# Kernel optimization log

Measured on AMD Instinct MI355X. Metric: run time of the kernel, lower is better.

## Reference

```python
import jax, jax.numpy as jnp
import numpy as np

N = 100000   # nodes
E = 1600000  # edges
F = 64       # input_features == output_features
BN_EPS = 1e-5


def _bn(x, gamma, beta):
    # torch BatchNorm1d (training mode): biased batch statistics
    mu = jnp.mean(x, axis=0)
    var = jnp.var(x, axis=0)
    return (x - mu) * jax.lax.rsqrt(var + BN_EPS) * gamma + beta


def setup_inputs() -> dict:
    key = jax.random.key(0)
    ks = jax.random.split(key, 16)
    s = 0.05
    inp = {
        'node_feats': jax.random.normal(ks[0], (N, F), jnp.float32),
        'edge_feats': jax.random.normal(ks[1], (E, F), jnp.float32),
        'src': jax.random.randint(ks[2], (E,), 0, N, jnp.int32),
        'dst': jax.random.randint(ks[3], (E,), 0, N, jnp.int32),
        # linear params: W [F_in, F_out], b [F_out]
        'W_src_gate': jax.random.normal(ks[4], (F, F), jnp.float32) * s,
        'b_src_gate': jnp.zeros((F,), jnp.float32),
        'W_dst_gate': jax.random.normal(ks[5], (F, F), jnp.float32) * s,
        'b_dst_gate': jnp.zeros((F,), jnp.float32),
        'W_edge_gate': jax.random.normal(ks[6], (F, F), jnp.float32) * s,
        'b_edge_gate': jnp.zeros((F,), jnp.float32),
        'W_src_update': jax.random.normal(ks[7], (F, F), jnp.float32) * s,
        'b_src_update': jnp.zeros((F,), jnp.float32),
        'W_dst_update': jax.random.normal(ks[8], (F, F), jnp.float32) * s,
        'b_dst_update': jnp.zeros((F,), jnp.float32),
        'bn_nodes_gamma': jnp.ones((F,), jnp.float32),
        'bn_nodes_beta': jnp.zeros((F,), jnp.float32),
        'bn_edges_gamma': jnp.ones((F,), jnp.float32),
        'bn_edges_beta': jnp.zeros((F,), jnp.float32),
    }
    return inp


def reference(node_feats, edge_feats, src, dst,
              W_src_gate, b_src_gate, W_dst_gate, b_dst_gate,
              W_edge_gate, b_edge_gate, W_src_update, b_src_update,
              W_dst_update, b_dst_update,
              bn_nodes_gamma, bn_nodes_beta, bn_edges_gamma, bn_edges_beta):
    # EdgeGatedGraphConv (arXiv:1711.07553), residual=True
    e_src = node_feats @ W_src_gate + b_src_gate          # [N,F]
    e_dst = node_feats @ W_dst_gate + b_dst_gate          # [N,F]
    # u_add_v gather + edge transform -> gate logits m [E,F]
    m = e_src[src] + e_dst[dst] + (edge_feats @ W_edge_gate + b_edge_gate)
    sigma = jax.nn.sigmoid(m)                             # [E,F]
    Bh = node_feats @ W_dst_update + b_dst_update         # [N,F]
    # u_mul_e message + scatter-sum to destination nodes
    sum_sigma_h = jax.ops.segment_sum(Bh[src] * sigma, dst, num_segments=node_feats.shape[0])
    sum_sigma = jax.ops.segment_sum(sigma, dst, num_segments=node_feats.shape[0])
    h = sum_sigma_h / (sum_sigma + 1e-6)                  # normalized aggregation
    x = node_feats @ W_src_update + b_src_update + h
    x = jax.nn.silu(_bn(x, bn_nodes_gamma, bn_nodes_beta))
    y = jax.nn.silu(_bn(m, bn_edges_gamma, bn_edges_beta))
    x = node_feats + x   # residual
    y = edge_feats + y   # residual
    return (x, y)
```

## Files before the change

### kernel.cpp

```cpp
#include <hip/hip_runtime.h>
#include <hip/hip_bf16.h>

typedef __attribute__((ext_vector_type(8))) __bf16 bf16x8;
typedef __attribute__((ext_vector_type(4))) float f32x4;

#define MFMA(a,b,c) __builtin_amdgcn_mfma_f32_16x16x32_bf16((a),(b),(c),0,0,0)

__device__ __forceinline__ bf16x8 cvt8(float4 a, float4 b){
  bf16x8 r;
  r[0]=(__bf16)a.x; r[1]=(__bf16)a.y; r[2]=(__bf16)a.z; r[3]=(__bf16)a.w;
  r[4]=(__bf16)b.x; r[5]=(__bf16)b.y; r[6]=(__bf16)b.z; r[7]=(__bf16)b.w;
  return r;
}

__global__ void zero_k(int4* __restrict__ p, int n4){
  int i = blockIdx.x*256 + threadIdx.x, st = gridDim.x*256;
  for (; i<n4; i+=st) p[i] = make_int4(0,0,0,0);
}

__global__ void wcvt(const float* __restrict__ W0, const float* __restrict__ W1,
                     const float* __restrict__ W2, const float* __restrict__ W3,
                     const float* __restrict__ W4, bf16x8* __restrict__ Wp){
  int tid = blockIdx.x*256 + threadIdx.x;
  if (tid >= 5*8*64) return;
  int lane = tid & 63, frag = (tid>>6)&7, m = tid>>9;
  const float* Ws[5] = {W0,W1,W2,W3,W4};
  const float* W = Ws[m];
  int kt = frag>>2, nt = frag&3, g = lane>>4, c = lane&15;
  bf16x8 v;
  #pragma unroll
  for (int j=0;j<8;j++) v[j] = (__bf16)W[(kt*32+g*8+j)*64 + nt*16 + c];
  Wp[tid] = v;
}

__global__ __launch_bounds__(256) void node_xform(
    const float* __restrict__ nf, const bf16x8* __restrict__ Wp,
    const float* __restrict__ b_su, const float* __restrict__ b_du,
    float* __restrict__ A_src, float* __restrict__ Bh, int ntiles)
{
  int lane = threadIdx.x & 63;
  int gw = blockIdx.x*4 + (threadIdx.x>>6);
  if (gw >= ntiles) return;
  int g = lane>>4, c = lane&15;
  long base = (long)gw*16;
  const float* rp = nf + (base + c)*64 + g*8;
  float4 a0 = *(const float4*)rp,      a1 = *(const float4*)(rp+4);
  float4 a2 = *(const float4*)(rp+32), a3 = *(const float4*)(rp+36);
  bf16x8 A0 = cvt8(a0,a1), A1 = cvt8(a2,a3);
  const float* biases[2] = {b_su,b_du};
  float* outs[2] = {A_src,Bh};
  const int mats[2] = {3,4};
  #pragma unroll
  for (int i=0;i<2;i++){
    #pragma unroll
    for (int nt=0;nt<4;nt++){
      f32x4 acc = {0.f,0.f,0.f,0.f};
      acc = MFMA(A0, Wp[(mats[i]*8+nt)*64+lane],   acc);
      acc = MFMA(A1, Wp[(mats[i]*8+4+nt)*64+lane], acc);
      int col = c + nt*16;
      float bb = biases[i][col];
      #pragma unroll
      for (int e=0;e<4;e++) outs[i][(base+4*g+e)*64 + col] = acc[e] + bb;
    }
  }
}

__global__ void hist_k(const int* __restrict__ dst, int* __restrict__ cnt, int E){
  int i = blockIdx.x*256 + threadIdx.x, st = gridDim.x*256;
  for (; i<E; i+=st) atomicAdd(&cnt[dst[i]], 1);
}

__global__ __launch_bounds__(1024) void scan_k(const int* __restrict__ cnt,
                                               int* __restrict__ row, int Nn){
  __shared__ int part[1024];
  int t = threadIdx.x;
  int C = (Nn + 1023) >> 10;
  int lo = t*C;
  int hi = lo + C; if (hi > Nn) hi = Nn;
  int s = 0;
  for (int i=lo; i<hi; i++) s += cnt[i];
  part[t] = s;
  __syncthreads();
  for (int off=1; off<1024; off<<=1){
    int v = part[t];
    int u = (t>=off) ? part[t-off] : 0;
    __syncthreads();
    part[t] = v + u;
    __syncthreads();
  }
  int excl = (t==0) ? 0 : part[t-1];
  for (int i=lo; i<hi; i++){ row[i] = excl; excl += cnt[i]; }
  if (t==1023) row[Nn] = excl;
}

__global__ void fill_k(const int* __restrict__ src, const int* __restrict__ dst,
                       const int* __restrict__ rowp, int* __restrict__ cnt2,
                       int2* __restrict__ pairs, int E){
  int i = blockIdx.x*256 + threadIdx.x, st = gridDim.x*256;
  for (; i<E; i+=st){
    int d = dst[i];
    int pos = rowp[d] + atomicAdd(&cnt2[d], 1);
    pairs[pos] = make_int2(i, src[i]);
  }
}

__global__ __launch_bounds__(256) void phaseA(
    const float* __restrict__ ef, const float* __restrict__ nf,
    const int* __restrict__ src, const int* __restrict__ dst,
    const float* __restrict__ b_sg, const float* __restrict__ b_dg,
    const float* __restrict__ b_eg,
    const bf16x8* __restrict__ Wp,
    __bf16* __restrict__ m16, int ntiles)
{
  __shared__ bf16x8 wl[24*64];
  {
    int t = threadIdx.x;
    #pragma unroll
    for (int i=0;i<6;i++){
      int idx = i*256 + t, fr = idx>>6, ln = idx&63;
      int mat = (fr<8) ? 2 : ((fr<16) ? 0 : 1);
      wl[idx] = Wp[(mat*8 + (fr&7))*64 + ln];
    }
  }
  __syncthreads();
  int lane = threadIdx.x & 63, g = lane>>4, c = lane&15;
  int gw = blockIdx.x*4 + (threadIdx.x>>6);
  int nw = gridDim.x*4;
  float bias[4];
  #pragma unroll
  for (int nt=0;nt<4;nt++){
    int col = c + 16*nt;
    bias[nt] = b_sg[col] + b_dg[col] + b_eg[col];
  }
  int sc = 0, dc = 0;
  if (gw < ntiles){ sc = src[(long)gw*16 + c]; dc = dst[(long)gw*16 + c]; }
  for (int tt=gw; tt<ntiles; tt+=nw){
    long base = (long)tt*16;
    int tn = tt + nw;
    int sn = sc, dn = dc;
    if (tn < ntiles){ sn = src[(long)tn*16 + c]; dn = dst[(long)tn*16 + c]; }
    const float* rpe = ef + (base+c)*64 + g*8;
    const float* rps = nf + (long)sc*64 + g*8;
    const float* rpd = nf + (long)dc*64 + g*8;
    float4 e0=*(const float4*)rpe,      e1=*(const float4*)(rpe+4);
    float4 e2=*(const float4*)(rpe+32), e3=*(const float4*)(rpe+36);
    float4 s0=*(const float4*)rps,      s1=*(const float4*)(rps+4);
    float4 s2=*(const float4*)(rps+32), s3=*(const float4*)(rps+36);
    float4 d0=*(const float4*)rpd,      d1=*(const float4*)(rpd+4);
    float4 d2=*(const float4*)(rpd+32), d3=*(const float4*)(rpd+36);
    bf16x8 AE0=cvt8(e0,e1), AE1=cvt8(e2,e3);
    bf16x8 AS0=cvt8(s0,s1), AS1=cvt8(s2,s3);
    bf16x8 AD0=cvt8(d0,d1), AD1=cvt8(d2,d3);
    #pragma unroll
    for (int nt=0;nt<4;nt++){
      f32x4 am = {0.f,0.f,0.f,0.f};
      am = MFMA(AE0, wl[(    nt)*64+lane], am);
      am = MFMA(AE1, wl[( 4+ nt)*64+lane], am);
      am = MFMA(AS0, wl[( 8+ nt)*64+lane], am);
      am = MFMA(AS1, wl[(12+ nt)*64+lane], am);
      am = MFMA(AD0, wl[(16+ nt)*64+lane], am);
      am = MFMA(AD1, wl[(20+ nt)*64+lane], am);
      int col = c + 16*nt;
      #pragma unroll
      for (int e=0;e<4;e++)
        m16[(base+4*g+e)*64 + col] = (__bf16)(am[e] + bias[nt]);
    }
    sc = sn; dc = dn;
  }
}

__global__ __launch_bounds__(256) void phaseB(
    const __bf16* __restrict__ m16, const int2* __restrict__ pairs,
    const float* __restrict__ Bh, const int* __restrict__ rowp,
    float* __restrict__ A_src,
    float* __restrict__ est, float* __restrict__ nst, int Nn)
{
  __shared__ float sst[256];
  sst[threadIdx.x] = 0.f;
  __syncthreads();
  int lane = threadIdx.x & 63, w = threadIdx.x>>6;
  int chunk = (Nn + gridDim.x - 1)/gridDim.x;
  int n0 = blockIdx.x*chunk;
  int n1 = n0 + chunk; if (n1 > Nn) n1 = Nn;
  float e1=0.f, e2=0.f, p1=0.f, p2=0.f;
  for (int n=n0+w; n<n1; n+=4){
    int r0 = rowp[n], r1 = rowp[n+1];
    float ssum=0.f, bsum=0.f;
    int r = r0;
    for (; r+4 <= r1; r+=4){
      int2 q0 = pairs[r],   q1 = pairs[r+1];
      int2 q2 = pairs[r+2], q3 = pairs[r+3];
      float mv0 = (float)m16[(long)q0.x*64 + lane];
      float mv1 = (float)m16[(long)q1.x*64 + lane];
      float mv2 = (float)m16[(long)q2.x*64 + lane];
      float mv3 = (float)m16[(long)q3.x*64 + lane];
      float bh0 = Bh[(long)q0.y*64 + lane];
      float bh1 = Bh[(long)q1.y*64 + lane];
      float bh2 = Bh[(long)q2.y*64 + lane];
      float bh3 = Bh[(long)q3.y*64 + lane];
      float sg0 = 1.f/(1.f+__expf(-mv0));
      float sg1 = 1.f/(1.f+__expf(-mv1));
      float sg2 = 1.f/(1.f+__expf(-mv2));
      float sg3 = 1.f/(1.f+__expf(-mv3));
      ssum += (sg0+sg1) + (sg2+sg3);
      bsum += (bh0*sg0 + bh1*sg1) + (bh2*sg2 + bh3*sg3);
      e1 += (mv0+mv1) + (mv2+mv3);
      e2 += (mv0*mv0 + mv1*mv1) + (mv2*mv2 + mv3*mv3);
    }
    for (; r < r1; ++r){
      int2 q0 = pairs[r];
      float mv0 = (float)m16[(long)q0.x*64 + lane];
      float bh0 = Bh[(long)q0.y*64 + lane];
      float sg0 = 1.f/(1.f+__expf(-mv0));
      ssum += sg0; bsum += bh0*sg0;
      e1 += mv0;   e2 += mv0*mv0;
    }
    long xi = (long)n*64 + lane;
    float xp = A_src[xi] + bsum/(ssum+1e-6f);
    A_src[xi] = xp;
    p1 += xp; p2 += xp*xp;
  }
  atomicAdd(&sst[lane],     e1);
  atomicAdd(&sst[64+lane],  e2);
  atomicAdd(&sst[128+lane], p1);
  atomicAdd(&sst[192+lane], p2);
  __syncthreads();
  int t = threadIdx.x;
  if (t < 128) atomicAdd(&est[t], sst[t]);
  else         atomicAdd(&nst[t-128], sst[t]);
}

__global__ __launch_bounds__(256) void node_final(
    const float* __restrict__ nf, const float* __restrict__ xpre,
    const float* __restrict__ nst, const float* __restrict__ gam,
    const float* __restrict__ bet, float* __restrict__ xo, int Nn)
{
  long tid = blockIdx.x*blockDim.x + threadIdx.x;
  long stride = (long)gridDim.x*blockDim.x;
  int col = (int)(tid & 63);
  float invN = 1.f/(float)Nn;
  float mu = nst[col]*invN;
  float var = nst[64+col]*invN - mu*mu;
  float rs = rsqrtf(var + 1e-5f);
  float aa = gam[col]*rs;
  float bb = bet[col] - mu*aa;
  long total = (long)Nn*64;
  for (long i=tid; i<total; i+=stride){
    float z = xpre[i]*aa + bb;
    xo[i] = nf[i] + z/(1.f+__expf(-z));
  }
}

__global__ __launch_bounds__(256) void edge_final(
    const __bf16* __restrict__ m16, const float* __restrict__ ef,
    const float* __restrict__ est, const float* __restrict__ gam,
    const float* __restrict__ bet, float* __restrict__ y, float invE, long E)
{
  int oct = threadIdx.x & 7;
  float aa[8], bb[8];
  #pragma unroll
  for (int j=0;j<8;j++){
    int col = oct*8 + j;
    float mu = est[col]*invE;
    float var = est[64+col]*invE - mu*mu;
    float rs = rsqrtf(var + 1e-5f);
    float ga = gam[col]*rs;
    aa[j] = ga; bb[j] = bet[col] - mu*ga;
  }
  long tid = (long)blockIdx.x*256 + threadIdx.x;
  long pstep = ((long)gridDim.x*256) >> 3;
  for (long p = tid>>3; p < E; p += pstep){
    bf16x8 mv = *(const bf16x8*)&m16[p*64 + oct*8];
    const float* rp = ef + p*64 + oct*8;
    float4 f0 = *(const float4*)rp, f1 = *(const float4*)(rp+4);
    float o[8];
    #pragma unroll
    for (int j=0;j<8;j++){
      float z = aa[j]*(float)mv[j] + bb[j];
      float ev = (j<4) ? ((const float*)&f0)[j] : ((const float*)&f1)[j-4];
      o[j] = ev + z/(1.f+__expf(-z));
    }
    float* yp = y + p*64 + oct*8;
    *(float4*)yp     = make_float4(o[0],o[1],o[2],o[3]);
    *(float4*)(yp+4) = make_float4(o[4],o[5],o[6],o[7]);
  }
}

extern "C" void kernel_launch(void* const* d_in, const int* in_sizes, int n_in,
                              void* d_out, int out_size, void* d_ws, size_t ws_size,
                              hipStream_t stream){
  const float* nf  = (const float*)d_in[0];
  const float* ef  = (const float*)d_in[1];
  const int*   src = (const int*)d_in[2];
  const int*   dst = (const int*)d_in[3];
  const float* W_sg=(const float*)d_in[4];  const float* b_sg=(const float*)d_in[5];
  const float* W_dg=(const float*)d_in[6];  const float* b_dg=(const float*)d_in[7];
  const float* W_eg=(const float*)d_in[8];  const float* b_eg=(const float*)d_in[9];
  const float* W_su=(const float*)d_in[10]; const float* b_su=(const float*)d_in[11];
  const float* W_du=(const float*)d_in[12]; const float* b_du=(const float*)d_in[13];
  const float* gn=(const float*)d_in[14];   const float* btn=(const float*)d_in[15];
  const float* ge=(const float*)d_in[16];   const float* bte=(const float*)d_in[17];

  int Nn = in_sizes[0]/64;
  int Ee = in_sizes[2];
  size_t Nf = (size_t)Nn*64;
  size_t Es = (size_t)Ee;

  float* ws    = (float*)d_ws;
  float* A_src = ws;
  float* Bh    = ws + Nf;
  __bf16* m16  = (__bf16*)(ws + 2*Nf);
  int2*  pairs = (int2*)(ws + 2*Nf + 32*Es);
  int*   cnt   = (int*)(pairs + Es);
  int*   cnt2  = cnt + Nn;
  float* est   = (float*)(cnt2 + Nn);
  float* nst   = est + 128;
  int*   rowp  = (int*)(nst + 128);
  size_t woff  = 2*Nf + 32*Es + 2*Es + 2*(size_t)Nn + 256 + (size_t)Nn + 1;
  woff = (woff + 15) & ~(size_t)15;
  bf16x8* Wp   = (bf16x8*)(ws + woff);

  float* xo = (float*)d_out;
  float* yo = xo + Nf;

  int nz4 = (int)((2*(size_t)Nn + 256) >> 2);
  zero_k<<<256,256,0,stream>>>((int4*)cnt, nz4);

  wcvt<<<10,256,0,stream>>>(W_sg,W_dg,W_eg,W_su,W_du,Wp);

  int ntn = Nn/16;
  node_xform<<<(ntn+3)/4,256,0,stream>>>(nf,Wp,b_su,b_du,A_src,Bh,ntn);
  hist_k<<<2048,256,0,stream>>>(dst,cnt,Ee);
  scan_k<<<1,1024,0,stream>>>(cnt,rowp,Nn);
  fill_k<<<2048,256,0,stream>>>(src,dst,rowp,cnt2,pairs,Ee);
  int nte = Ee/16;
  phaseA<<<4096,256,0,stream>>>(ef,nf,src,dst,b_sg,b_dg,b_eg,Wp,m16,nte);
  phaseB<<<4096,256,0,stream>>>(m16,pairs,Bh,rowp,A_src,est,nst,Nn);
  node_final<<<2048,256,0,stream>>>(nf,A_src,nst,gn,btn,xo,Nn);
  edge_final<<<2048,256,0,stream>>>(m16,ef,est,ge,bte,yo,
                                    1.f/(float)Ee,(long)Ee);
}
```

Before: 968.8 us.

## Transpose phaseA MFMA so edge outputs store as packed contiguous bf16 runs

phaseA now computes the transposed product (W^T as the A operand, edge features as B), so each lane holds four consecutive feature columns of one edge. It can then write one 8-byte packed store instead of four scattered 2-byte stores. A second pre-swizzled weight buffer is built in wcvt so phaseA can copy it straight into LDS. phaseB's gather loop is unrolled to 8 edges with all loads issued first for more memory-level parallelism, and edge_final gets twice as many blocks.

```diff
diff --git a/kernel.cpp b/kernel.cpp
--- a/kernel.cpp
+++ b/kernel.cpp
@@ -18,19 +18,33 @@
   for (; i<n4; i+=st) p[i] = make_int4(0,0,0,0);
 }
 
-__global__ void wcvt(const float* __restrict__ W0, const float* __restrict__ W1,
-                     const float* __restrict__ W2, const float* __restrict__ W3,
-                     const float* __restrict__ W4, bf16x8* __restrict__ Wp){
+__global__ void wcvt(const float* __restrict__ W_sg, const float* __restrict__ W_dg,
+                     const float* __restrict__ W_eg, const float* __restrict__ W_su,
+                     const float* __restrict__ W_du,
+                     bf16x8* __restrict__ Wp, bf16x8* __restrict__ Wq){
   int tid = blockIdx.x*256 + threadIdx.x;
-  if (tid >= 5*8*64) return;
-  int lane = tid & 63, frag = (tid>>6)&7, m = tid>>9;
-  const float* Ws[5] = {W0,W1,W2,W3,W4};
-  const float* W = Ws[m];
-  int kt = frag>>2, nt = frag&3, g = lane>>4, c = lane&15;
-  bf16x8 v;
-  #pragma unroll
-  for (int j=0;j<8;j++) v[j] = (__bf16)W[(kt*32+g*8+j)*64 + nt*16 + c];
-  Wp[tid] = v;
+  if (tid >= 2560 + 1536) return;
+  int lane = tid & 63, g = lane>>4, c = lane&15;
+  if (tid < 2560){
+    int frag = (tid>>6)&7, m = tid>>9;
+    const float* Ws[5] = {W_sg, W_dg, W_eg, W_su, W_du};
+    const float* W = Ws[m];
+    int kt = frag>>2, nt = frag&3;
+    bf16x8 v;
+    #pragma unroll
+    for (int j=0;j<8;j++) v[j] = (__bf16)W[(kt*32+g*8+j)*64 + nt*16 + c];
+    Wp[tid] = v;
+  } else {
+    int t2 = tid - 2560;
+    int frag = (t2>>6)&7, m = t2>>9;
+    const float* Ws[3] = {W_eg, W_sg, W_dg};
+    const float* W = Ws[m];
+    int mt = frag>>1, kh = frag&1;
+    bf16x8 v;
+    #pragma unroll
+    for (int j=0;j<8;j++) v[j] = (__bf16)W[(kh*32+g*8+j)*64 + mt*16 + c];
+    Wq[t2] = v;
+  }
 }
 
 __global__ __launch_bounds__(256) void node_xform(
@@ -109,29 +123,27 @@
     const int* __restrict__ src, const int* __restrict__ dst,
     const float* __restrict__ b_sg, const float* __restrict__ b_dg,
     const float* __restrict__ b_eg,
-    const bf16x8* __restrict__ Wp,
+    const bf16x8* __restrict__ Wq,
     __bf16* __restrict__ m16, int ntiles)
 {
   __shared__ bf16x8 wl[24*64];
   {
     int t = threadIdx.x;
     #pragma unroll
-    for (int i=0;i<6;i++){
-      int idx = i*256 + t, fr = idx>>6, ln = idx&63;
-      int mat = (fr<8) ? 2 : ((fr<16) ? 0 : 1);
-      wl[idx] = Wp[(mat*8 + (fr&7))*64 + ln];
-    }
+    for (int i=0;i<6;i++) wl[i*256+t] = Wq[i*256+t];
   }
   __syncthreads();
   int lane = threadIdx.x & 63, g = lane>>4, c = lane&15;
   int gw = blockIdx.x*4 + (threadIdx.x>>6);
   int nw = gridDim.x*4;
-  float bias[4];
+  float bias2[4][4];
   #pragma unroll
-  for (int nt=0;nt<4;nt++){
-    int col = c + 16*nt;
-    bias[nt] = b_sg[col] + b_dg[col] + b_eg[col];
-  }
+  for (int mt=0;mt<4;mt++)
+    #pragma unroll
+    for (int e=0;e<4;e++){
+      int f = mt*16 + 4*g + e;
+      bias2[mt][e] = b_sg[f] + b_dg[f] + b_eg[f];
+    }
   int sc = 0, dc = 0;
   if (gw < ntiles){ sc = src[(long)gw*16 + c]; dc = dst[(long)gw*16 + c]; }
   for (int tt=gw; tt<ntiles; tt+=nw){
@@ -148,22 +160,22 @@
     float4 s2=*(const float4*)(rps+32), s3=*(const float4*)(rps+36);
     float4 d0=*(const float4*)rpd,      d1=*(const float4*)(rpd+4);
     float4 d2=*(const float4*)(rpd+32), d3=*(const float4*)(rpd+36);
-    bf16x8 AE0=cvt8(e0,e1), AE1=cvt8(e2,e3);
-    bf16x8 AS0=cvt8(s0,s1), AS1=cvt8(s2,s3);
-    bf16x8 AD0=cvt8(d0,d1), AD1=cvt8(d2,d3);
-    #pragma unroll
-    for (int nt=0;nt<4;nt++){
+    bf16x8 BE0=cvt8(e0,e1), BE1=cvt8(e2,e3);
+    bf16x8 BS0=cvt8(s0,s1), BS1=cvt8(s2,s3);
+    bf16x8 BD0=cvt8(d0,d1), BD1=cvt8(d2,d3);
+    #pragma unroll
+    for (int mt=0;mt<4;mt++){
       f32x4 am = {0.f,0.f,0.f,0.f};
-      am = MFMA(AE0, wl[(    nt)*64+lane], am);
-      am = MFMA(AE1, wl[( 4+ nt)*64+lane], am);
-      am = MFMA(AS0, wl[( 8+ nt)*64+lane], am);
-      am = MFMA(AS1, wl[(12+ nt)*64+lane], am);
-      am = MFMA(AD0, wl[(16+ nt)*64+lane], am);
-      am = MFMA(AD1, wl[(20+ nt)*64+lane], am);
-      int col = c + 16*nt;
-      #pragma unroll
-      for (int e=0;e<4;e++)
-        m16[(base+4*g+e)*64 + col] = (__bf16)(am[e] + bias[nt]);
+      am = MFMA(wl[((0*4+mt)*2+0)*64+lane], BE0, am);
+      am = MFMA(wl[((0*4+mt)*2+1)*64+lane], BE1, am);
+      am = MFMA(wl[((1*4+mt)*2+0)*64+lane], BS0, am);
+      am = MFMA(wl[((1*4+mt)*2+1)*64+lane], BS1, am);
+      am = MFMA(wl[((2*4+mt)*2+0)*64+lane], BD0, am);
+      am = MFMA(wl[((2*4+mt)*2+1)*64+lane], BD1, am);
+      union { __bf16 h[4]; uint2 u; } pk;
+      #pragma unroll
+      for (int e=0;e<4;e++) pk.h[e] = (__bf16)(am[e] + bias2[mt][e]);
+      *(uint2*)(m16 + (base+c)*64 + mt*16 + 4*g) = pk.u;
     }
     sc = sn; dc = dn;
   }
@@ -187,25 +199,21 @@
     int r0 = rowp[n], r1 = rowp[n+1];
     float ssum=0.f, bsum=0.f;
     int r = r0;
-    for (; r+4 <= r1; r+=4){
-      int2 q0 = pairs[r],   q1 = pairs[r+1];
-      int2 q2 = pairs[r+2], q3 = pairs[r+3];
-      float mv0 = (float)m16[(long)q0.x*64 + lane];
-      float mv1 = (float)m16[(long)q1.x*64 + lane];
-      float mv2 = (float)m16[(long)q2.x*64 + lane];
-      float mv3 = (float)m16[(long)q3.x*64 + lane];
-      float bh0 = Bh[(long)q0.y*64 + lane];
-      float bh1 = Bh[(long)q1.y*64 + lane];
-      float bh2 = Bh[(long)q2.y*64 + lane];
-      float bh3 = Bh[(long)q3.y*64 + lane];
-      float sg0 = 1.f/(1.f+__expf(-mv0));
-      float sg1 = 1.f/(1.f+__expf(-mv1));
-      float sg2 = 1.f/(1.f+__expf(-mv2));
-      float sg3 = 1.f/(1.f+__expf(-mv3));
-      ssum += (sg0+sg1) + (sg2+sg3);
-      bsum += (bh0*sg0 + bh1*sg1) + (bh2*sg2 + bh3*sg3);
-      e1 += (mv0+mv1) + (mv2+mv3);
-      e2 += (mv0*mv0 + mv1*mv1) + (mv2*mv2 + mv3*mv3);
+    for (; r+8 <= r1; r+=8){
+      int2 q[8];
+      #pragma unroll
+      for (int j=0;j<8;j++) q[j] = pairs[r+j];
+      float mv[8], bh[8];
+      #pragma unroll
+      for (int j=0;j<8;j++) mv[j] = (float)m16[(long)q[j].x*64 + lane];
+      #pragma unroll
+      for (int j=0;j<8;j++) bh[j] = Bh[(long)q[j].y*64 + lane];
+      #pragma unroll
+      for (int j=0;j<8;j++){
+        float sg = 1.f/(1.f+__expf(-mv[j]));
+        ssum += sg; bsum += bh[j]*sg;
+        e1 += mv[j]; e2 += mv[j]*mv[j];
+      }
     }
     for (; r < r1; ++r){
       int2 q0 = pairs[r];
@@ -319,6 +327,7 @@
   size_t woff  = 2*Nf + 32*Es + 2*Es + 2*(size_t)Nn + 256 + (size_t)Nn + 1;
   woff = (woff + 15) & ~(size_t)15;
   bf16x8* Wp   = (bf16x8*)(ws + woff);
+  bf16x8* Wq   = Wp + 2560;
 
   float* xo = (float*)d_out;
   float* yo = xo + Nf;
@@ -326,7 +335,7 @@
   int nz4 = (int)((2*(size_t)Nn + 256) >> 2);
   zero_k<<<256,256,0,stream>>>((int4*)cnt, nz4);
 
-  wcvt<<<10,256,0,stream>>>(W_sg,W_dg,W_eg,W_su,W_du,Wp);
+  wcvt<<<16,256,0,stream>>>(W_sg,W_dg,W_eg,W_su,W_du,Wp,Wq);
 
   int ntn = Nn/16;
   node_xform<<<(ntn+3)/4,256,0,stream>>>(nf,Wp,b_su,b_du,A_src,Bh,ntn);
@@ -334,9 +343,9 @@
   scan_k<<<1,1024,0,stream>>>(cnt,rowp,Nn);
   fill_k<<<2048,256,0,stream>>>(src,dst,rowp,cnt2,pairs,Ee);
   int nte = Ee/16;
-  phaseA<<<4096,256,0,stream>>>(ef,nf,src,dst,b_sg,b_dg,b_eg,Wp,m16,nte);
+  phaseA<<<4096,256,0,stream>>>(ef,nf,src,dst,b_sg,b_dg,b_eg,Wq,m16,nte);
   phaseB<<<4096,256,0,stream>>>(m16,pairs,Bh,rowp,A_src,est,nst,Nn);
   node_final<<<2048,256,0,stream>>>(nf,A_src,nst,gn,btn,xo,Nn);
-  edge_final<<<2048,256,0,stream>>>(m16,ef,est,ge,bte,yo,
+  edge_final<<<4096,256,0,stream>>>(m16,ef,est,ge,bte,yo,
                                     1.f/(float)Ee,(long)Ee);
 }
```

Result: no change. 962.4 us, median of 2 (-0.7%).
